# Kernel optimization log

Hardware: AMD Instinct MI355X
Metric: run time of the kernel (lower is better)

Reference implementation:

```python
import jax, jax.numpy as jnp
import numpy as np

B, S, D = 4, 2048, 1024

def _xavier(key, shape):
    bound = float(np.sqrt(6.0 / (shape[0] + shape[1])))
    return jax.random.uniform(key, shape, dtype=jnp.float32, minval=-bound, maxval=bound)

def setup_inputs() -> dict:
    key = jax.random.key(0)
    k0, k1, k2, k3 = jax.random.split(key, 4)
    return {
        "embeddings": jax.random.normal(k0, (B, S, D), dtype=jnp.float32),
        "W_Q": _xavier(k1, (D, D)),
        "W_K": _xavier(k2, (D, D)),
        "W_V": _xavier(k3, (D, D)),
    }

def reference(embeddings, W_Q, W_K, W_V):
    _, seq_len, d = embeddings.shape
    Q = embeddings @ W_Q                      # [B,S,D]
    K = embeddings @ W_K
    V = embeddings @ W_V
    scale = 1.0 / jnp.sqrt(jnp.float32(d))
    scores = jnp.einsum('bqd,bkd->bqk', Q, K) * scale   # [B,S,S]
    causal = jnp.tril(jnp.ones((seq_len, seq_len), dtype=bool))
    scores = jnp.where(causal[None, :, :], scores, -jnp.inf)
    probs = jax.nn.softmax(scores, axis=-1)
    return jnp.einsum('bqk,bkd->bqd', probs, V)
```

## Files before the change

### kernel.cpp

```cpp
#include <hip/hip_runtime.h>
#include <hip/hip_bf16.h>

#define BSZ 4
#define SEQ 2048
#define DIM 1024

typedef __attribute__((ext_vector_type(8))) short bf16x8;
typedef __attribute__((ext_vector_type(4))) float floatx4;

__device__ __forceinline__ unsigned short f2bf(float x) {
  union { float f; unsigned int u; } v; v.f = x;
  unsigned int r = v.u + 0x7fffu + ((v.u >> 16) & 1u);
  return (unsigned short)(r >> 16);
}

template <typename T> __device__ __forceinline__ void store_c(T* p, float v);
template <> __device__ __forceinline__ void store_c<float>(float* p, float v) { *p = v; }
template <> __device__ __forceinline__ void store_c<unsigned short>(unsigned short* p, float v) { *p = f2bf(v); }

__global__ __launch_bounds__(256) void cast_e(const float* __restrict__ in,
                                              unsigned short* __restrict__ out, int n) {
  int i = (blockIdx.x * 256 + threadIdx.x) * 4;
  if (i >= n) return;
  float4 v = *(const float4*)(in + i);
  ushort4 o;
  o.x = f2bf(v.x); o.y = f2bf(v.y); o.z = f2bf(v.z); o.w = f2bf(v.w);
  *(ushort4*)(out + i) = o;
}

__global__ __launch_bounds__(256) void transpose_w(const float* __restrict__ Wq,
                                                   const float* __restrict__ Wk,
                                                   const float* __restrict__ Wv,
                                                   unsigned short* __restrict__ WtQK,
                                                   unsigned short* __restrict__ WtV) {
  __shared__ float tile[32][33];
  int z = blockIdx.z;
  const float* W = (z == 0) ? Wq : (z == 1) ? Wk : Wv;
  unsigned short* dst = (z == 2) ? WtV : WtQK;
  int row_off = (z == 1) ? 1024 : 0;
  int n0 = blockIdx.x * 32, k0 = blockIdx.y * 32;
  int tx = threadIdx.x, ty = threadIdx.y;
  for (int r = ty; r < 32; r += 8)
    tile[r][tx] = W[(size_t)(k0 + r) * DIM + n0 + tx];
  __syncthreads();
  for (int r = ty; r < 32; r += 8)
    dst[(size_t)(row_off + n0 + r) * DIM + k0 + tx] = f2bf(tile[tx][r]);
}

template <typename OutT, int MODE>
__global__ __launch_bounds__(256) void gemm_nt(
    const unsigned short* __restrict__ A, int lda, long long strideA,
    const unsigned short* __restrict__ B, int ldb, long long strideB,
    OutT* __restrict__ C, int ldc, long long strideC,
    int Kdim, float scale, float* __restrict__ rowsum) {
  int m0 = blockIdx.y * 128;
  int n0 = blockIdx.x * 128;
  if (MODE == 1 && n0 > m0) return;
  int Keff = (MODE == 2) ? min(Kdim, m0 + 128) : Kdim;
  A += (long long)blockIdx.z * strideA;
  B += (long long)blockIdx.z * strideB;
  C += (long long)blockIdx.z * strideC;
  if (MODE != 0) rowsum += (size_t)blockIdx.z * SEQ;

  __shared__ __align__(16) unsigned short As[128][72];
  __shared__ __align__(16) unsigned short Bs[128][72];

  int tid = threadIdx.x;
  int lane = tid & 63;
  int wid = tid >> 6;
  int wm = (wid >> 1) * 64, wn = (wid & 1) * 64;
  int lr = lane & 15, lq = lane >> 4;

  int row = tid >> 3;
  int kc = (tid & 7) * 8;

  const unsigned short* Ab = A + (size_t)(m0 + row) * lda + kc;
  const unsigned short* Bb = B + (size_t)(n0 + row) * ldb + kc;
  size_t la = (size_t)32 * lda, lb = (size_t)32 * ldb;

  uint4 ra0 = *(const uint4*)(Ab);
  uint4 ra1 = *(const uint4*)(Ab + la);
  uint4 ra2 = *(const uint4*)(Ab + 2 * la);
  uint4 ra3 = *(const uint4*)(Ab + 3 * la);
  uint4 rb0 = *(const uint4*)(Bb);
  uint4 rb1 = *(const uint4*)(Bb + lb);
  uint4 rb2 = *(const uint4*)(Bb + 2 * lb);
  uint4 rb3 = *(const uint4*)(Bb + 3 * lb);

  floatx4 acc[4][4] = {};

  for (int k0 = 0; k0 < Keff; k0 += 64) {
    __syncthreads();
    *(uint4*)&As[row][kc]      = ra0;
    *(uint4*)&As[row + 32][kc] = ra1;
    *(uint4*)&As[row + 64][kc] = ra2;
    *(uint4*)&As[row + 96][kc] = ra3;
    *(uint4*)&Bs[row][kc]      = rb0;
    *(uint4*)&Bs[row + 32][kc] = rb1;
    *(uint4*)&Bs[row + 64][kc] = rb2;
    *(uint4*)&Bs[row + 96][kc] = rb3;
    if (k0 + 64 < Keff) {
      const unsigned short* An = Ab + k0 + 64;
      const unsigned short* Bn = Bb + k0 + 64;
      ra0 = *(const uint4*)(An);
      ra1 = *(const uint4*)(An + la);
      ra2 = *(const uint4*)(An + 2 * la);
      ra3 = *(const uint4*)(An + 3 * la);
      rb0 = *(const uint4*)(Bn);
      rb1 = *(const uint4*)(Bn + lb);
      rb2 = *(const uint4*)(Bn + 2 * lb);
      rb3 = *(const uint4*)(Bn + 3 * lb);
    }
    __syncthreads();
#pragma unroll
    for (int kk = 0; kk < 64; kk += 32) {
      bf16x8 af[4], bfr[4];
      int kl = kk + lq * 8;
#pragma unroll
      for (int i = 0; i < 4; i++) af[i] = *(const bf16x8*)&As[wm + i * 16 + lr][kl];
#pragma unroll
      for (int j = 0; j < 4; j++) bfr[j] = *(const bf16x8*)&Bs[wn + j * 16 + lr][kl];
#pragma unroll
      for (int i = 0; i < 4; i++)
#pragma unroll
        for (int j = 0; j < 4; j++)
          acc[i][j] = __builtin_amdgcn_mfma_f32_16x16x32_bf16(af[i], bfr[j], acc[i][j], 0, 0, 0);
    }
  }

  if constexpr (MODE == 1) {
#pragma unroll
    for (int i = 0; i < 4; i++) {
      int rbase = m0 + wm + i * 16 + lq * 4;
      float s0 = 0.f, s1 = 0.f, s2 = 0.f, s3 = 0.f;
#pragma unroll
      for (int j = 0; j < 4; j++) {
        int col = n0 + wn + j * 16 + lr;
        float e0 = (col <= rbase + 0) ? __expf(acc[i][j][0] * scale) : 0.0f;
        float e1 = (col <= rbase + 1) ? __expf(acc[i][j][1] * scale) : 0.0f;
        float e2 = (col <= rbase + 2) ? __expf(acc[i][j][2] * scale) : 0.0f;
        float e3 = (col <= rbase + 3) ? __expf(acc[i][j][3] * scale) : 0.0f;
        store_c(&C[(size_t)(rbase + 0) * ldc + col], e0);
        store_c(&C[(size_t)(rbase + 1) * ldc + col], e1);
        store_c(&C[(size_t)(rbase + 2) * ldc + col], e2);
        store_c(&C[(size_t)(rbase + 3) * ldc + col], e3);
        s0 += e0; s1 += e1; s2 += e2; s3 += e3;
      }
#pragma unroll
      for (int m = 1; m < 16; m <<= 1) {
        s0 += __shfl_xor(s0, m, 64);
        s1 += __shfl_xor(s1, m, 64);
        s2 += __shfl_xor(s2, m, 64);
        s3 += __shfl_xor(s3, m, 64);
      }
      if (lr == 0) {
        atomicAdd(&rowsum[rbase + 0], s0);
        atomicAdd(&rowsum[rbase + 1], s1);
        atomicAdd(&rowsum[rbase + 2], s2);
        atomicAdd(&rowsum[rbase + 3], s3);
      }
    }
  } else if constexpr (MODE == 2) {
#pragma unroll
    for (int i = 0; i < 4; i++) {
      int rbase = m0 + wm + i * 16 + lq * 4;
      float i0 = 1.0f / rowsum[rbase + 0];
      float i1 = 1.0f / rowsum[rbase + 1];
      float i2 = 1.0f / rowsum[rbase + 2];
      float i3 = 1.0f / rowsum[rbase + 3];
#pragma unroll
      for (int j = 0; j < 4; j++) {
        int col = n0 + wn + j * 16 + lr;
        store_c(&C[(size_t)(rbase + 0) * ldc + col], acc[i][j][0] * i0);
        store_c(&C[(size_t)(rbase + 1) * ldc + col], acc[i][j][1] * i1);
        store_c(&C[(size_t)(rbase + 2) * ldc + col], acc[i][j][2] * i2);
        store_c(&C[(size_t)(rbase + 3) * ldc + col], acc[i][j][3] * i3);
      }
    }
  } else {
#pragma unroll
    for (int i = 0; i < 4; i++) {
      int rbase = m0 + wm + i * 16 + lq * 4;
#pragma unroll
      for (int j = 0; j < 4; j++) {
        int col = n0 + wn + j * 16 + lr;
#pragma unroll
        for (int r = 0; r < 4; r++)
          store_c(&C[(size_t)(rbase + r) * ldc + col], acc[i][j][r] * scale);
      }
    }
  }
}

extern "C" void kernel_launch(void* const* d_in, const int* in_sizes, int n_in,
                              void* d_out, int out_size, void* d_ws, size_t ws_size,
                              hipStream_t stream) {
  const float* E  = (const float*)d_in[0];
  const float* Wq = (const float*)d_in[1];
  const float* Wk = (const float*)d_in[2];
  const float* Wv = (const float*)d_in[3];
  float* out = (float*)d_out;

  char* ws = (char*)d_ws;
  size_t off = 0;
  auto alloc = [&](size_t bytes) {
    void* p = ws + off;
    off += (bytes + 255) & ~(size_t)255;
    return p;
  };
  const size_t M_ALL = (size_t)BSZ * SEQ;
  unsigned short* Ebf  = (unsigned short*)alloc(M_ALL * DIM * 2);
  unsigned short* WtQK = (unsigned short*)alloc((size_t)2 * DIM * DIM * 2);
  unsigned short* WtV  = (unsigned short*)alloc((size_t)DIM * DIM * 2);
  unsigned short* QK   = (unsigned short*)alloc(M_ALL * 2 * DIM * 2);
  unsigned short* Vt   = (unsigned short*)alloc((size_t)DIM * M_ALL * 2);
  unsigned short* ExpS = (unsigned short*)alloc((size_t)BSZ * SEQ * SEQ * 2);
  float*          Rsum = (float*)alloc((size_t)BSZ * SEQ * 4);

  int nE = (int)(M_ALL * DIM);
  cast_e<<<dim3(nE / (256 * 4)), dim3(256), 0, stream>>>(E, Ebf, nE);
  transpose_w<<<dim3(32, 32, 3), dim3(32, 8), 0, stream>>>(Wq, Wk, Wv, WtQK, WtV);

  gemm_nt<unsigned short, 0><<<dim3(16, 64, 1), dim3(256), 0, stream>>>(
      Ebf, DIM, 0, WtQK, DIM, 0, QK, 2 * DIM, 0, DIM, 1.0f, nullptr);

  gemm_nt<unsigned short, 0><<<dim3(64, 8, 1), dim3(256), 0, stream>>>(
      WtV, DIM, 0, Ebf, DIM, 0, Vt, (int)M_ALL, 0, DIM, 1.0f, nullptr);

  hipMemsetAsync(Rsum, 0, (size_t)BSZ * SEQ * 4, stream);

  gemm_nt<unsigned short, 1><<<dim3(16, 16, BSZ), dim3(256), 0, stream>>>(
      QK, 2 * DIM, (long long)SEQ * 2 * DIM,
      QK + DIM, 2 * DIM, (long long)SEQ * 2 * DIM,
      ExpS, SEQ, (long long)SEQ * SEQ,
      DIM, 0.03125f , Rsum);

  gemm_nt<float, 2><<<dim3(8, 16, BSZ), dim3(256), 0, stream>>>(
      ExpS, SEQ, (long long)SEQ * SEQ,
      Vt, (int)M_ALL, (long long)SEQ,
      out, DIM, (long long)SEQ * DIM,
      SEQ, 1.0f, Rsum);
}
```

Before: 249.9 us.

## Deepen GEMM register prefetch to two stages and compact causal tile grid

```diff
diff --git a/kernel.cpp b/kernel.cpp
--- a/kernel.cpp
+++ b/kernel.cpp
@@ -1,5 +1,6 @@
 #include <hip/hip_runtime.h>
 #include <hip/hip_bf16.h>
+#include <math.h>
 
 #define BSZ 4
 #define SEQ 2048
@@ -47,15 +48,45 @@
     dst[(size_t)(row_off + n0 + r) * DIM + k0 + tx] = f2bf(tile[tx][r]);
 }
 
+#define COMPUTE_TILE()                                                          \
+  {                                                                             \
+    _Pragma("unroll")                                                           \
+    for (int kk = 0; kk < 64; kk += 32) {                                       \
+      bf16x8 af[4], bfr[4];                                                     \
+      int kl = kk + lq * 8;                                                     \
+      _Pragma("unroll")                                                         \
+      for (int i = 0; i < 4; i++) af[i] = *(const bf16x8*)&As[wm + i * 16 + lr][kl];  \
+      _Pragma("unroll")                                                         \
+      for (int j = 0; j < 4; j++) bfr[j] = *(const bf16x8*)&Bs[wn + j * 16 + lr][kl]; \
+      _Pragma("unroll")                                                         \
+      for (int i = 0; i < 4; i++)                                               \
+        _Pragma("unroll")                                                       \
+        for (int j = 0; j < 4; j++)                                             \
+          acc[i][j] = __builtin_amdgcn_mfma_f32_16x16x32_bf16(af[i], bfr[j], acc[i][j], 0, 0, 0); \
+    }                                                                           \
+  }
+
 template <typename OutT, int MODE>
 __global__ __launch_bounds__(256) void gemm_nt(
     const unsigned short* __restrict__ A, int lda, long long strideA,
     const unsigned short* __restrict__ B, int ldb, long long strideB,
     OutT* __restrict__ C, int ldc, long long strideC,
     int Kdim, float scale, float* __restrict__ rowsum) {
-  int m0 = blockIdx.y * 128;
-  int n0 = blockIdx.x * 128;
-  if (MODE == 1 && n0 > m0) return;
+  int m0, n0;
+  if constexpr (MODE == 1) {
+    int t = blockIdx.x;
+    int mt = (int)((sqrtf(8.0f * (float)t + 1.0f) - 1.0f) * 0.5f);
+    int nt = t - (mt * (mt + 1)) / 2;
+    if (nt < 0) { mt--; nt = t - (mt * (mt + 1)) / 2; }
+    else if (nt > mt) { mt++; nt = t - (mt * (mt + 1)) / 2; }
+    m0 = mt * 128; n0 = nt * 128;
+  } else if constexpr (MODE == 2) {
+    m0 = (gridDim.y - 1 - blockIdx.y) * 128;
+    n0 = blockIdx.x * 128;
+  } else {
+    m0 = blockIdx.y * 128;
+    n0 = blockIdx.x * 128;
+  }
   int Keff = (MODE == 2) ? min(Kdim, m0 + 128) : Kdim;
   A += (long long)blockIdx.z * strideA;
   B += (long long)blockIdx.z * strideB;
@@ -86,10 +117,18 @@
   uint4 rb1 = *(const uint4*)(Bb + lb);
   uint4 rb2 = *(const uint4*)(Bb + 2 * lb);
   uint4 rb3 = *(const uint4*)(Bb + 3 * lb);
+  uint4 rc0 = *(const uint4*)(Ab + 64);
+  uint4 rc1 = *(const uint4*)(Ab + la + 64);
+  uint4 rc2 = *(const uint4*)(Ab + 2 * la + 64);
+  uint4 rc3 = *(const uint4*)(Ab + 3 * la + 64);
+  uint4 rd0 = *(const uint4*)(Bb + 64);
+  uint4 rd1 = *(const uint4*)(Bb + lb + 64);
+  uint4 rd2 = *(const uint4*)(Bb + 2 * lb + 64);
+  uint4 rd3 = *(const uint4*)(Bb + 3 * lb + 64);
 
   floatx4 acc[4][4] = {};
 
-  for (int k0 = 0; k0 < Keff; k0 += 64) {
+  for (int k0 = 0; k0 < Keff; k0 += 128) {
     __syncthreads();
     *(uint4*)&As[row][kc]      = ra0;
     *(uint4*)&As[row + 32][kc] = ra1;
@@ -99,9 +138,9 @@
     *(uint4*)&Bs[row + 32][kc] = rb1;
     *(uint4*)&Bs[row + 64][kc] = rb2;
     *(uint4*)&Bs[row + 96][kc] = rb3;
-    if (k0 + 64 < Keff) {
-      const unsigned short* An = Ab + k0 + 64;
-      const unsigned short* Bn = Bb + k0 + 64;
+    if (k0 + 128 < Keff) {
+      const unsigned short* An = Ab + k0 + 128;
+      const unsigned short* Bn = Bb + k0 + 128;
       ra0 = *(const uint4*)(An);
       ra1 = *(const uint4*)(An + la);
       ra2 = *(const uint4*)(An + 2 * la);
@@ -112,20 +151,31 @@
       rb3 = *(const uint4*)(Bn + 3 * lb);
     }
     __syncthreads();
-#pragma unroll
-    for (int kk = 0; kk < 64; kk += 32) {
-      bf16x8 af[4], bfr[4];
-      int kl = kk + lq * 8;
-#pragma unroll
-      for (int i = 0; i < 4; i++) af[i] = *(const bf16x8*)&As[wm + i * 16 + lr][kl];
-#pragma unroll
-      for (int j = 0; j < 4; j++) bfr[j] = *(const bf16x8*)&Bs[wn + j * 16 + lr][kl];
-#pragma unroll
-      for (int i = 0; i < 4; i++)
-#pragma unroll
-        for (int j = 0; j < 4; j++)
-          acc[i][j] = __builtin_amdgcn_mfma_f32_16x16x32_bf16(af[i], bfr[j], acc[i][j], 0, 0, 0);
-    }
+    COMPUTE_TILE();
+
+    __syncthreads();
+    *(uint4*)&As[row][kc]      = rc0;
+    *(uint4*)&As[row + 32][kc] = rc1;
+    *(uint4*)&As[row + 64][kc] = rc2;
+    *(uint4*)&As[row + 96][kc] = rc3;
+    *(uint4*)&Bs[row][kc]      = rd0;
+    *(uint4*)&Bs[row + 32][kc] = rd1;
+    *(uint4*)&Bs[row + 64][kc] = rd2;
+    *(uint4*)&Bs[row + 96][kc] = rd3;
+    if (k0 + 192 < Keff) {
+      const unsigned short* An = Ab + k0 + 192;
+      const unsigned short* Bn = Bb + k0 + 192;
+      rc0 = *(const uint4*)(An);
+      rc1 = *(const uint4*)(An + la);
+      rc2 = *(const uint4*)(An + 2 * la);
+      rc3 = *(const uint4*)(An + 3 * la);
+      rd0 = *(const uint4*)(Bn);
+      rd1 = *(const uint4*)(Bn + lb);
+      rd2 = *(const uint4*)(Bn + 2 * lb);
+      rd3 = *(const uint4*)(Bn + 3 * lb);
+    }
+    __syncthreads();
+    COMPUTE_TILE();
   }
 
   if constexpr (MODE == 1) {
@@ -229,7 +279,7 @@
 
   hipMemsetAsync(Rsum, 0, (size_t)BSZ * SEQ * 4, stream);
 
-  gemm_nt<unsigned short, 1><<<dim3(16, 16, BSZ), dim3(256), 0, stream>>>(
+  gemm_nt<unsigned short, 1><<<dim3(136, 1, BSZ), dim3(256), 0, stream>>>(
       QK, 2 * DIM, (long long)SEQ * 2 * DIM,
       QK + DIM, 2 * DIM, (long long)SEQ * 2 * DIM,
       ExpS, SEQ, (long long)SEQ * SEQ,
```

Result: no change. 253.0 us (+1.2%).

## Merge QK and V projections into one launch, compact causal grid, reverse PV order

Applied to the files above, without the earlier changes.

```diff
diff --git a/kernel.cpp b/kernel.cpp
--- a/kernel.cpp
+++ b/kernel.cpp
@@ -47,20 +47,25 @@
     dst[(size_t)(row_off + n0 + r) * DIM + k0 + tx] = f2bf(tile[tx][r]);
 }
 
-template <typename OutT, int MODE>
-__global__ __launch_bounds__(256) void gemm_nt(
-    const unsigned short* __restrict__ A, int lda, long long strideA,
-    const unsigned short* __restrict__ B, int ldb, long long strideB,
-    OutT* __restrict__ C, int ldc, long long strideC,
-    int Kdim, float scale, float* __restrict__ rowsum) {
-  int m0 = blockIdx.y * 128;
-  int n0 = blockIdx.x * 128;
-  if (MODE == 1 && n0 > m0) return;
-  int Keff = (MODE == 2) ? min(Kdim, m0 + 128) : Kdim;
-  A += (long long)blockIdx.z * strideA;
-  B += (long long)blockIdx.z * strideB;
-  C += (long long)blockIdx.z * strideC;
-  if (MODE != 0) rowsum += (size_t)blockIdx.z * SEQ;
+__global__ __launch_bounds__(256) void proj_dual(
+    const unsigned short* __restrict__ Ebf,
+    const unsigned short* __restrict__ WtQK,
+    const unsigned short* __restrict__ WtV,
+    unsigned short* __restrict__ QKo,
+    unsigned short* __restrict__ Vt) {
+  const unsigned short *A, *B;
+  unsigned short* C;
+  int lda, ldb, ldc, m0, n0;
+  int x = blockIdx.x;
+  if (x < 1024) {
+    m0 = (x >> 4) * 128; n0 = (x & 15) * 128;
+    A = Ebf; lda = DIM; B = WtQK; ldb = DIM; C = QKo; ldc = 2 * DIM;
+  } else {
+    x -= 1024;
+    m0 = (x >> 6) * 128; n0 = (x & 63) * 128;
+    A = WtV; lda = DIM; B = Ebf; ldb = DIM; C = Vt; ldc = BSZ * SEQ;
+  }
+  const int Keff = DIM;
 
   __shared__ __align__(16) unsigned short As[128][72];
   __shared__ __align__(16) unsigned short Bs[128][72];
@@ -70,7 +75,6 @@
   int wid = tid >> 6;
   int wm = (wid >> 1) * 64, wn = (wid & 1) * 64;
   int lr = lane & 15, lq = lane >> 4;
-
   int row = tid >> 3;
   int kc = (tid & 7) * 8;
 
@@ -128,6 +132,107 @@
     }
   }
 
+#pragma unroll
+  for (int i = 0; i < 4; i++) {
+    int rbase = m0 + wm + i * 16 + lq * 4;
+#pragma unroll
+    for (int j = 0; j < 4; j++) {
+      int col = n0 + wn + j * 16 + lr;
+#pragma unroll
+      for (int r = 0; r < 4; r++)
+        C[(size_t)(rbase + r) * ldc + col] = f2bf(acc[i][j][r]);
+    }
+  }
+}
+
+template <typename OutT, int MODE>
+__global__ __launch_bounds__(256) void gemm_nt(
+    const unsigned short* __restrict__ A, int lda, long long strideA,
+    const unsigned short* __restrict__ B, int ldb, long long strideB,
+    OutT* __restrict__ C, int ldc, long long strideC,
+    int Kdim, float scale, float* __restrict__ rowsum) {
+  int m0, n0;
+  if constexpr (MODE == 1) {
+    int t = blockIdx.x;
+    int mt = 0;
+    while (((mt + 1) * (mt + 2)) / 2 <= t) mt++;
+    int nt = t - (mt * (mt + 1)) / 2;
+    m0 = mt * 128; n0 = nt * 128;
+  } else {
+    m0 = (gridDim.y - 1 - blockIdx.y) * 128;
+    n0 = blockIdx.x * 128;
+  }
+  int Keff = (MODE == 2) ? min(Kdim, m0 + 128) : Kdim;
+  A += (long long)blockIdx.z * strideA;
+  B += (long long)blockIdx.z * strideB;
+  C += (long long)blockIdx.z * strideC;
+  rowsum += (size_t)blockIdx.z * SEQ;
+
+  __shared__ __align__(16) unsigned short As[128][72];
+  __shared__ __align__(16) unsigned short Bs[128][72];
+
+  int tid = threadIdx.x;
+  int lane = tid & 63;
+  int wid = tid >> 6;
+  int wm = (wid >> 1) * 64, wn = (wid & 1) * 64;
+  int lr = lane & 15, lq = lane >> 4;
+  int row = tid >> 3;
+  int kc = (tid & 7) * 8;
+
+  const unsigned short* Ab = A + (size_t)(m0 + row) * lda + kc;
+  const unsigned short* Bb = B + (size_t)(n0 + row) * ldb + kc;
+  size_t la = (size_t)32 * lda, lb = (size_t)32 * ldb;
+
+  uint4 ra0 = *(const uint4*)(Ab);
+  uint4 ra1 = *(const uint4*)(Ab + la);
+  uint4 ra2 = *(const uint4*)(Ab + 2 * la);
+  uint4 ra3 = *(const uint4*)(Ab + 3 * la);
+  uint4 rb0 = *(const uint4*)(Bb);
+  uint4 rb1 = *(const uint4*)(Bb + lb);
+  uint4 rb2 = *(const uint4*)(Bb + 2 * lb);
+  uint4 rb3 = *(const uint4*)(Bb + 3 * lb);
+
+  floatx4 acc[4][4] = {};
+
+  for (int k0 = 0; k0 < Keff; k0 += 64) {
+    __syncthreads();
+    *(uint4*)&As[row][kc]      = ra0;
+    *(uint4*)&As[row + 32][kc] = ra1;
+    *(uint4*)&As[row + 64][kc] = ra2;
+    *(uint4*)&As[row + 96][kc] = ra3;
+    *(uint4*)&Bs[row][kc]      = rb0;
+    *(uint4*)&Bs[row + 32][kc] = rb1;
+    *(uint4*)&Bs[row + 64][kc] = rb2;
+    *(uint4*)&Bs[row + 96][kc] = rb3;
+    if (k0 + 64 < Keff) {
+      const unsigned short* An = Ab + k0 + 64;
+      const unsigned short* Bn = Bb + k0 + 64;
+      ra0 = *(const uint4*)(An);
+      ra1 = *(const uint4*)(An + la);
+      ra2 = *(const uint4*)(An + 2 * la);
+      ra3 = *(const uint4*)(An + 3 * la);
+      rb0 = *(const uint4*)(Bn);
+      rb1 = *(const uint4*)(Bn + lb);
+      rb2 = *(const uint4*)(Bn + 2 * lb);
+      rb3 = *(const uint4*)(Bn + 3 * lb);
+    }
+    __syncthreads();
+#pragma unroll
+    for (int kk = 0; kk < 64; kk += 32) {
+      bf16x8 af[4], bfr[4];
+      int kl = kk + lq * 8;
+#pragma unroll
+      for (int i = 0; i < 4; i++) af[i] = *(const bf16x8*)&As[wm + i * 16 + lr][kl];
+#pragma unroll
+      for (int j = 0; j < 4; j++) bfr[j] = *(const bf16x8*)&Bs[wn + j * 16 + lr][kl];
+#pragma unroll
+      for (int i = 0; i < 4; i++)
+#pragma unroll
+        for (int j = 0; j < 4; j++)
+          acc[i][j] = __builtin_amdgcn_mfma_f32_16x16x32_bf16(af[i], bfr[j], acc[i][j], 0, 0, 0);
+    }
+  }
+
   if constexpr (MODE == 1) {
 #pragma unroll
     for (int i = 0; i < 4; i++) {
@@ -160,7 +265,7 @@
         atomicAdd(&rowsum[rbase + 3], s3);
       }
     }
-  } else if constexpr (MODE == 2) {
+  } else {
 #pragma unroll
     for (int i = 0; i < 4; i++) {
       int rbase = m0 + wm + i * 16 + lq * 4;
@@ -175,18 +280,6 @@
         store_c(&C[(size_t)(rbase + 1) * ldc + col], acc[i][j][1] * i1);
         store_c(&C[(size_t)(rbase + 2) * ldc + col], acc[i][j][2] * i2);
         store_c(&C[(size_t)(rbase + 3) * ldc + col], acc[i][j][3] * i3);
-      }
-    }
-  } else {
-#pragma unroll
-    for (int i = 0; i < 4; i++) {
-      int rbase = m0 + wm + i * 16 + lq * 4;
-#pragma unroll
-      for (int j = 0; j < 4; j++) {
-        int col = n0 + wn + j * 16 + lr;
-#pragma unroll
-        for (int r = 0; r < 4; r++)
-          store_c(&C[(size_t)(rbase + r) * ldc + col], acc[i][j][r] * scale);
       }
     }
   }
@@ -220,16 +313,11 @@
   int nE = (int)(M_ALL * DIM);
   cast_e<<<dim3(nE / (256 * 4)), dim3(256), 0, stream>>>(E, Ebf, nE);
   transpose_w<<<dim3(32, 32, 3), dim3(32, 8), 0, stream>>>(Wq, Wk, Wv, WtQK, WtV);
-
-  gemm_nt<unsigned short, 0><<<dim3(16, 64, 1), dim3(256), 0, stream>>>(
-      Ebf, DIM, 0, WtQK, DIM, 0, QK, 2 * DIM, 0, DIM, 1.0f, nullptr);
-
-  gemm_nt<unsigned short, 0><<<dim3(64, 8, 1), dim3(256), 0, stream>>>(
-      WtV, DIM, 0, Ebf, DIM, 0, Vt, (int)M_ALL, 0, DIM, 1.0f, nullptr);
-
   hipMemsetAsync(Rsum, 0, (size_t)BSZ * SEQ * 4, stream);
 
-  gemm_nt<unsigned short, 1><<<dim3(16, 16, BSZ), dim3(256), 0, stream>>>(
+  proj_dual<<<dim3(1536), dim3(256), 0, stream>>>(Ebf, WtQK, WtV, QK, Vt);
+
+  gemm_nt<unsigned short, 1><<<dim3(136, 1, BSZ), dim3(256), 0, stream>>>(
       QK, 2 * DIM, (long long)SEQ * 2 * DIM,
       QK + DIM, 2 * DIM, (long long)SEQ * 2 * DIM,
       ExpS, SEQ, (long long)SEQ * SEQ,
```

New measurement: 241.7 us. 3.3% less time.
